# Optimization experiments

Measured on AMD Instinct MI355X. Metric: run time of the kernel, lower is better.

## Reference

```python
import jax, jax.numpy as jnp
import numpy as np

H = 300  # hidden size hardcoded in the module
VX = 32000
VY = 32000
NX, NY, B = 128, 128, 256


def setup_inputs() -> dict:
    key = jax.random.key(0)
    ks = jax.random.split(key, 10)
    s = 1.0 / np.sqrt(H)
    x = jax.random.randint(ks[0], (NX, B), 0, VX)
    y = jax.random.randint(ks[1], (NY, B), 0, VY)
    # padding_idx=0: zero the pad row of each embedding table
    enc_emb = jax.random.normal(ks[2], (VX, H), jnp.float32).at[0].set(0.0)
    encW = jax.random.uniform(ks[3], (H, H), jnp.float32, -s, s)
    encb = jax.random.uniform(ks[4], (H,), jnp.float32, -s, s)
    dec_emb = jax.random.normal(ks[5], (VY, H), jnp.float32).at[0].set(0.0)
    decW = jax.random.uniform(ks[6], (H, H), jnp.float32, -s, s)
    decb = jax.random.uniform(ks[7], (H,), jnp.float32, -s, s)
    outW = jax.random.uniform(ks[8], (VY, H), jnp.float32, -s, s)
    outb = jax.random.uniform(ks[9], (VY,), jnp.float32, -s, s)
    return {"x": x, "y": y, "enc_emb": enc_emb, "encW": encW, "encb": encb,
            "dec_emb": dec_emb, "decW": decW, "decb": decb,
            "outW": outW, "outb": outb}


def reference(x, y, enc_emb, encW, encb, dec_emb, decW, decb, outW, outb):
    # Encoder: Elman recurrence h = relu(e_x[i] + W h + b)
    e_x = enc_emb[x]                                  # [NX, B, H]
    h0 = jnp.zeros((x.shape[1], H), e_x.dtype)        # h=0 broadcast over batch

    def enc_step(h, ex):
        return jax.nn.relu(ex + h @ encW.T + encb), None

    h, _ = jax.lax.scan(enc_step, h0, e_x)

    # Decoder: teacher-forced recurrence with per-step mean cross-entropy
    e_y = dec_emb[y]                                  # [NY, B, H]

    def dec_step(h, inp):
        ey, tgt = inp
        h = jax.nn.relu(ey + h @ decW.T + decb)
        logits = h @ outW.T + outb                    # [B, VY]
        logp = jax.nn.log_softmax(logits, axis=-1)
        ce = -jnp.mean(jnp.take_along_axis(logp, tgt[:, None], axis=-1))
        return h, ce

    _, ces = jax.lax.scan(dec_step, h, (e_y[:-1], y[1:]))
    return jnp.sum(ces)
```

## Files before the change

### kernel.cpp

```cpp
#include <hip/hip_runtime.h>
#include <hip/hip_bf16.h>
#include <stdint.h>

typedef unsigned short u16;
typedef unsigned char u8;
typedef float f32x4 __attribute__((ext_vector_type(4)));
typedef float f32x2 __attribute__((ext_vector_type(2)));
typedef _Float16 f16x2 __attribute__((ext_vector_type(2)));
typedef _Float16 f16x8 __attribute__((ext_vector_type(8)));

#define H      300
#define KP     320
#define BATCH  256
#define NX     128
#define NY     128
#define VY     32000
#define NPAD   32768
#define MROWS  32512


#define OWS_OFF   0UL
#define OWS_BYTES ((unsigned long)NPAD * KP)
#define OWS_PAD   131072UL
#define A8_OFF    (OWS_OFF + OWS_BYTES + OWS_PAD)
#define A8_BYTES  ((unsigned long)MROWS * KP)
#define WTE_OFF   (A8_OFF + A8_BYTES)
#define WT_BYTES  (320UL * KP * 4)
#define WTD_OFF   (WTE_OFF + WT_BYTES)
#define OBP_OFF   (WTD_OFF + WT_BYTES)
#define OBP_BYTES ((unsigned long)NPAD * 4)
#define SE_OFF    (OBP_OFF + OBP_BYTES)
#define SE_BYTES  ((unsigned long)MROWS * 4)

#define ASYNC_COPY16(dst_lds, src_glb)                                          \
    __builtin_amdgcn_global_load_lds(                                           \
        (const __attribute__((address_space(1))) unsigned int*)(src_glb),       \
        (__attribute__((address_space(3))) unsigned int*)(dst_lds), 16, 0, 0)

__global__ __launch_bounds__(256) void k0_prep(const float* __restrict__ outW,
                                               const float* __restrict__ encW,
                                               const float* __restrict__ decW,
                                               const float* __restrict__ outb,
                                               u8* __restrict__ ows,
                                               float* __restrict__ eob,
                                               float* __restrict__ wte,
                                               float* __restrict__ wtd) {
    long id = (long)blockIdx.x * 256 + threadIdx.x;
    const long n1 = (long)NPAD * KP / 4;
    if (id < n1) {
        int v = (int)(id / 80), k4 = (int)(id % 80) * 4;
        float4 f = {0.f, 0.f, 0.f, 0.f};
        if (v < VY && k4 < H) f = *(const float4*)&outW[(long)v * H + k4];
        int w = __builtin_amdgcn_cvt_pk_fp8_f32(f.x, f.y, 0, false);
        w = __builtin_amdgcn_cvt_pk_fp8_f32(f.z, f.w, w, true);
        long dst = (long)(v >> 6) * 20480 + (k4 >> 5) * 2048 + ((v >> 4) & 3) * 512
                 + (v & 15) * 8 + ((k4 >> 3) & 3) * 128 + (k4 & 7);
        *(unsigned int*)(ows + dst) = (unsigned int)w;
        return;
    }
    long id2 = id - n1;
    if (id2 < NPAD) {
        eob[id2] = (id2 < VY) ? __expf(outb[id2]) : 0.f;
        return;
    }
    id2 -= NPAD;
    if (id2 < 320L * KP) {
        int k = (int)(id2 / KP), j = (int)(id2 % KP);
        wte[id2] = (k < H && j < H) ? encW[j * H + k] : 0.f;
        return;
    }
    id2 -= 320L * KP;
    if (id2 < 320L * KP) {
        int k = (int)(id2 / KP), j = (int)(id2 % KP);
        wtd[id2] = (k < H && j < H) ? decW[j * H + k] : 0.f;
    }
}

__global__ __launch_bounds__(640) void k1_rnn(const int* __restrict__ x,
                                              const int* __restrict__ y,
                                              const float* __restrict__ enc_emb,
                                              const float* __restrict__ dec_emb,
                                              const float* __restrict__ encb,
                                              const float* __restrict__ decb,
                                              const float* __restrict__ wte,
                                              const float* __restrict__ wtd,
                                              u8* __restrict__ A8) {
    const int tid = threadIdx.x;
    const int s = tid / 160;
    const int j = tid - s * 160;
    const int b = blockIdx.x;

    __shared__ __align__(16) _Float16 hh[320];
    __shared__ float part[1280];
    __shared__ __align__(4) u8 a8row[320];

    for (int i = tid; i < 320; i += 640) hh[i] = (_Float16)0.f;

    const bool comb = (tid < 320);
    const int jc = tid;
    const float be = (comb && jc < H) ? encb[jc] : 0.f;
    const float bd = (comb && jc < H) ? decb[jc] : 0.f;

    f16x2 wa[40], wc[40];
#pragma unroll
    for (int kk = 0; kk < 40; ++kk) {
        int k0 = s * 80 + 2 * kk;
        wa[kk] = (f16x2){(_Float16)wte[k0 * KP + j],       (_Float16)wte[(k0 + 1) * KP + j]};
        wc[kk] = (f16x2){(_Float16)wte[k0 * KP + j + 160], (_Float16)wte[(k0 + 1) * KP + j + 160]};
    }

    int idx_n = x[BATCH + b];
    float e_cur = 0.f;
    if (comb && jc < H) e_cur = enc_emb[(long)x[b] * H + jc];
    __syncthreads();

    const f16x8* hb8 = (const f16x8*)&hh[s * 80];

    for (int t = 0; t < NX; ++t) {
        int idx_n2 = x[min(t + 2, NX - 1) * BATCH + b];
        float e_nx = 0.f;
        if (comb && jc < H && t + 1 < NX) e_nx = enc_emb[(long)idx_n * H + jc];

        float p0 = 0.f, p1 = 0.f;
#pragma unroll
        for (int i = 0; i < 10; ++i) {
            f16x8 hv = hb8[i];
            f16x2 q0 = {hv[0], hv[1]}, q1 = {hv[2], hv[3]};
            f16x2 q2 = {hv[4], hv[5]}, q3 = {hv[6], hv[7]};
            p0 = __builtin_amdgcn_fdot2(wa[4 * i + 0], q0, p0, false);
            p1 = __builtin_amdgcn_fdot2(wc[4 * i + 0], q0, p1, false);
            p0 = __builtin_amdgcn_fdot2(wa[4 * i + 1], q1, p0, false);
            p1 = __builtin_amdgcn_fdot2(wc[4 * i + 1], q1, p1, false);
            p0 = __builtin_amdgcn_fdot2(wa[4 * i + 2], q2, p0, false);
            p1 = __builtin_amdgcn_fdot2(wc[4 * i + 2], q2, p1, false);
            p0 = __builtin_amdgcn_fdot2(wa[4 * i + 3], q3, p0, false);
            p1 = __builtin_amdgcn_fdot2(wc[4 * i + 3], q3, p1, false);
        }
        part[s * 320 + j] = p0;
        part[s * 320 + 160 + j] = p1;
        __syncthreads();
        if (comb) {
            float v = part[jc] + part[320 + jc] + part[640 + jc] + part[960 + jc] + be + e_cur;
            hh[jc] = (_Float16)fmaxf(v, 0.f);
        }
        __syncthreads();
        e_cur = e_nx; idx_n = idx_n2;
    }

#pragma unroll
    for (int kk = 0; kk < 40; ++kk) {
        int k0 = s * 80 + 2 * kk;
        wa[kk] = (f16x2){(_Float16)wtd[k0 * KP + j],       (_Float16)wtd[(k0 + 1) * KP + j]};
        wc[kk] = (f16x2){(_Float16)wtd[k0 * KP + j + 160], (_Float16)wtd[(k0 + 1) * KP + j + 160]};
    }

    idx_n = y[BATCH + b];
    e_cur = 0.f;
    if (comb && jc < H) e_cur = dec_emb[(long)y[b] * H + jc];

    for (int t = 0; t < NY - 1; ++t) {
        int idx_n2 = y[min(t + 2, NY - 1) * BATCH + b];
        float e_nx = 0.f;
        if (comb && jc < H && t + 1 < NY - 1) e_nx = dec_emb[(long)idx_n * H + jc];

        float p0 = 0.f, p1 = 0.f;
#pragma unroll
        for (int i = 0; i < 10; ++i) {
            f16x8 hv = hb8[i];
            f16x2 q0 = {hv[0], hv[1]}, q1 = {hv[2], hv[3]};
            f16x2 q2 = {hv[4], hv[5]}, q3 = {hv[6], hv[7]};
            p0 = __builtin_amdgcn_fdot2(wa[4 * i + 0], q0, p0, false);
            p1 = __builtin_amdgcn_fdot2(wc[4 * i + 0], q0, p1, false);
            p0 = __builtin_amdgcn_fdot2(wa[4 * i + 1], q1, p0, false);
            p1 = __builtin_amdgcn_fdot2(wc[4 * i + 1], q1, p1, false);
            p0 = __builtin_amdgcn_fdot2(wa[4 * i + 2], q2, p0, false);
            p1 = __builtin_amdgcn_fdot2(wc[4 * i + 2], q2, p1, false);
            p0 = __builtin_amdgcn_fdot2(wa[4 * i + 3], q3, p0, false);
            p1 = __builtin_amdgcn_fdot2(wc[4 * i + 3], q3, p1, false);
        }
        part[s * 320 + j] = p0;
        part[s * 320 + 160 + j] = p1;
        __syncthreads();
        if (comb) {
            float v = part[jc] + part[320 + jc] + part[640 + jc] + part[960 + jc] + bd + e_cur;
            v = fmaxf(v, 0.f);
            hh[jc] = (_Float16)v;
            int pk = __builtin_amdgcn_cvt_pk_fp8_f32(v, v, 0, false);
            a8row[jc] = (u8)(pk & 0xff);
        }
        __syncthreads();
        if (tid < 80)
            ((unsigned int*)(A8 + (long)(t * BATCH + b) * KP))[tid] =
                ((const unsigned int*)a8row)[tid];
        e_cur = e_nx; idx_n = idx_n2;
    }
}

__global__ __launch_bounds__(256, 2) void k2_gemm(const u8* __restrict__ A8,
                                                  const u8* __restrict__ OWS,
                                                  const float* __restrict__ eob,
                                                  float* __restrict__ sumexp) {
    const int tid = threadIdx.x;
    const int lane = tid & 63, wave = tid >> 6;
    const int lane16 = lane & 15, quad = lane >> 4;
    const int bid = blockIdx.x;
    const int cg8 = bid & 7;
    const int cs  = (bid >> 3) & 3;
    const int rb  = bid >> 5;
    const int colbase = cg8 * 4096 + cs * 1024;
    const long tile0 = (long)(colbase >> 6);

    __shared__ __align__(16) u8 bt[2][20480];

    long a[4][10];
    {
        const u8* abase = A8 + ((long)rb * 256 + wave * 64 + lane16) * KP + quad * 8;
#pragma unroll
        for (int rt = 0; rt < 4; ++rt)
#pragma unroll
            for (int ks = 0; ks < 10; ++ks)
                a[rt][ks] = *(const long*)(abase + rt * 16 * KP + ks * 32);
    }

    {
        const u8* src = OWS + tile0 * 20480 + (wave << 10) + (lane << 4);
        u8* dst = &bt[0][wave << 10];
#pragma unroll
        for (int r = 0; r < 5; ++r)
            ASYNC_COPY16(dst + r * 4096, src + r * 4096);
    }
    __syncthreads();

    float rsum[16];
#pragma unroll
    for (int i = 0; i < 16; ++i) rsum[i] = 0.f;

    for (int ct = 0; ct < 16; ++ct) {
        const u8* bb = &bt[ct & 1][0];

        if (ct < 15) {
            const u8* src = OWS + (tile0 + ct + 1) * 20480 + (wave << 10) + (lane << 4);
            u8* dst = &bt[(ct + 1) & 1][wave << 10];
#pragma unroll
            for (int r = 0; r < 5; ++r)
                ASYNC_COPY16(dst + r * 4096, src + r * 4096);
        }

        f32x4 acc[4][4];
#pragma unroll
        for (int p = 0; p < 4; ++p)
#pragma unroll
            for (int q = 0; q < 4; ++q) acc[p][q] = (f32x4){0.f, 0.f, 0.f, 0.f};

#pragma unroll
        for (int ks = 0; ks < 10; ++ks) {
            long bfr[4];
#pragma unroll
            for (int tc = 0; tc < 4; ++tc)
                bfr[tc] = *(const long*)(bb + ks * 2048 + tc * 512 + lane * 8);
#pragma unroll
            for (int rt = 0; rt < 4; ++rt)
#pragma unroll
                for (int tc = 0; tc < 4; ++tc)
                    acc[rt][tc] = __builtin_amdgcn_mfma_f32_16x16x32_fp8_fp8(
                        a[rt][ks], bfr[tc], acc[rt][tc], 0, 0, 0);
        }

        int cb = colbase + ct * 64;
#pragma unroll
        for (int tc = 0; tc < 4; ++tc) {
            float eb = eob[cb + tc * 16 + lane16];
#pragma unroll
            for (int rt = 0; rt < 4; ++rt)
#pragma unroll
                for (int i = 0; i < 4; ++i)
                    rsum[rt * 4 + i] += __expf(acc[rt][tc][i]) * eb;
        }

        __syncthreads();
    }

#pragma unroll
    for (int m = 1; m < 16; m <<= 1)
#pragma unroll
        for (int i = 0; i < 16; ++i) rsum[i] += __shfl_xor(rsum[i], m, 64);
    if (lane16 == 0) {
        float* sp = &sumexp[(long)rb * 256 + wave * 64];
#pragma unroll
        for (int rt = 0; rt < 4; ++rt)
#pragma unroll
            for (int i = 0; i < 4; ++i)
                atomicAdd(&sp[rt * 16 + quad * 4 + i], rsum[rt * 4 + i]);
    }
}

__global__ __launch_bounds__(256) void k3_ce(const u8* __restrict__ A8,
                                             const u8* __restrict__ OWS,
                                             const float* __restrict__ outb,
                                             const float* __restrict__ sumexp,
                                             const int* __restrict__ y,
                                             float* __restrict__ out) {
    const int wave = threadIdx.x >> 6, lane = threadIdx.x & 63;
    const int r = blockIdx.x * 4 + wave;
    const int t = r >> 8, b = r & 255;
    const int tgt = y[(t + 1) * BATCH + b];
    float s = 0.f;
    if (lane < 40) {
        unsigned long long av = *(const unsigned long long*)(A8 + (long)r * KP + lane * 8);
        long wdst = (long)(tgt >> 6) * 20480 + (lane >> 2) * 2048
                  + ((tgt >> 4) & 3) * 512 + (tgt & 15) * 8 + (lane & 3) * 128;
        unsigned long long wv = *(const unsigned long long*)(OWS + wdst);
        unsigned int a4 = (unsigned int)av, a4h = (unsigned int)(av >> 32);
        unsigned int w4 = (unsigned int)wv, w4h = (unsigned int)(wv >> 32);
        f32x2 al = __builtin_amdgcn_cvt_pk_f32_fp8(a4, false);
        f32x2 ah = __builtin_amdgcn_cvt_pk_f32_fp8(a4, true);
        f32x2 wl = __builtin_amdgcn_cvt_pk_f32_fp8(w4, false);
        f32x2 wh = __builtin_amdgcn_cvt_pk_f32_fp8(w4, true);
        s += al[0] * wl[0] + al[1] * wl[1] + ah[0] * wh[0] + ah[1] * wh[1];
        al = __builtin_amdgcn_cvt_pk_f32_fp8(a4h, false);
        ah = __builtin_amdgcn_cvt_pk_f32_fp8(a4h, true);
        wl = __builtin_amdgcn_cvt_pk_f32_fp8(w4h, false);
        wh = __builtin_amdgcn_cvt_pk_f32_fp8(w4h, true);
        s += al[0] * wl[0] + al[1] * wl[1] + ah[0] * wh[0] + ah[1] * wh[1];
    }
#pragma unroll
    for (int m = 1; m < 64; m <<= 1) s += __shfl_xor(s, m, 64);
    __shared__ float part[4];
    if (lane == 0) part[wave] = logf(sumexp[r]) - (s + outb[tgt]);
    __syncthreads();
    if (threadIdx.x == 0) {
        float tot = part[0] + part[1] + part[2] + part[3];
        atomicAdd(out, tot * (1.0f / 256.0f));
    }
}

extern "C" void kernel_launch(void* const* d_in, const int* in_sizes, int n_in,
                              void* d_out, int out_size, void* d_ws, size_t ws_size,
                              hipStream_t stream) {
    (void)in_sizes; (void)n_in; (void)out_size; (void)ws_size;
    const int*   x       = (const int*)d_in[0];
    const int*   y       = (const int*)d_in[1];
    const float* enc_emb = (const float*)d_in[2];
    const float* encW    = (const float*)d_in[3];
    const float* encb    = (const float*)d_in[4];
    const float* dec_emb = (const float*)d_in[5];
    const float* decW    = (const float*)d_in[6];
    const float* decb    = (const float*)d_in[7];
    const float* outW    = (const float*)d_in[8];
    const float* outb    = (const float*)d_in[9];

    char* ws = (char*)d_ws;
    u8* ows  = (u8*)(ws + OWS_OFF);
    u8* A8   = (u8*)(ws + A8_OFF);
    float* wte    = (float*)(ws + WTE_OFF);
    float* wtd    = (float*)(ws + WTD_OFF);
    float* eob    = (float*)(ws + OBP_OFF);
    float* sumexp = (float*)(ws + SE_OFF);

    hipMemsetAsync(sumexp, 0, SE_BYTES, stream);
    hipMemsetAsync(d_out, 0, sizeof(float), stream);

    long n0 = (long)NPAD * KP / 4 + NPAD + 2L * 320 * KP;
    k0_prep<<<(int)((n0 + 255) / 256), 256, 0, stream>>>(outW, encW, decW, outb,
                                                         ows, eob, wte, wtd);
    k1_rnn<<<256, 640, 0, stream>>>(x, y, enc_emb, dec_emb, encb, decb, wte, wtd, A8);
    k2_gemm<<<127 * 32, 256, 0, stream>>>(A8, ows, eob, sumexp);
    k3_ce<<<8128, 256, 0, stream>>>(A8, ows, outb, sumexp, y, (float*)d_out);
}
```

Baseline: 962.7 us.

## Software-pipeline k2_gemm: overlap exp epilogue of previous tile with next MFMA tile

The column-tile loop in k2_gemm now uses two accumulator sets, so the exp-and-sum epilogue for tile ct-1 runs after the MFMA chain of tile ct. The two phases can then interleave and hide transcendental latency behind matrix work, and the barrier moves to the start of each step. In exchange, register pressure rises from a second 64-float accumulator set, which under launch_bounds(256,2) may cause spills or lower occupancy. An unused shared rowsum array is also added.

```diff
diff --git a/kernel.cpp b/kernel.cpp
--- a/kernel.cpp
+++ b/kernel.cpp
@@ -212,6 +212,9 @@
 
     __shared__ __align__(16) u8 bt[2][20480];
 
+    __shared__ float rowsum[64];
+    if (tid < 64) rowsum[tid] = 0.f;
+
     long a[4][10];
     {
         const u8* abase = A8 + ((long)rb * 256 + wave * 64 + lane16) * KP + quad * 8;
@@ -229,44 +232,66 @@
         for (int r = 0; r < 5; ++r)
             ASYNC_COPY16(dst + r * 4096, src + r * 4096);
     }
-    __syncthreads();
 
     float rsum[16];
 #pragma unroll
     for (int i = 0; i < 16; ++i) rsum[i] = 0.f;
 
-    for (int ct = 0; ct < 16; ++ct) {
-        const u8* bb = &bt[ct & 1][0];
-
-        if (ct < 15) {
-            const u8* src = OWS + (tile0 + ct + 1) * 20480 + (wave << 10) + (lane << 4);
-            u8* dst = &bt[(ct + 1) & 1][wave << 10];
-#pragma unroll
-            for (int r = 0; r < 5; ++r)
-                ASYNC_COPY16(dst + r * 4096, src + r * 4096);
-        }
-
-        f32x4 acc[4][4];
-#pragma unroll
-        for (int p = 0; p < 4; ++p)
-#pragma unroll
-            for (int q = 0; q < 4; ++q) acc[p][q] = (f32x4){0.f, 0.f, 0.f, 0.f};
-
-#pragma unroll
-        for (int ks = 0; ks < 10; ++ks) {
-            long bfr[4];
-#pragma unroll
-            for (int tc = 0; tc < 4; ++tc)
-                bfr[tc] = *(const long*)(bb + ks * 2048 + tc * 512 + lane * 8);
-#pragma unroll
-            for (int rt = 0; rt < 4; ++rt)
-#pragma unroll
-                for (int tc = 0; tc < 4; ++tc)
-                    acc[rt][tc] = __builtin_amdgcn_mfma_f32_16x16x32_fp8_fp8(
-                        a[rt][ks], bfr[tc], acc[rt][tc], 0, 0, 0);
-        }
-
-        int cb = colbase + ct * 64;
+    f32x4 accA[4][4], accB[4][4];
+
+#define DO_CT(CUR, PRV, CT, DO_EPI)                                             \
+    {                                                                           \
+        __syncthreads();                                                        \
+        if ((CT) < 15) {                                                        \
+            const u8* src = OWS + (tile0 + (CT) + 1) * 20480                    \
+                          + (wave << 10) + (lane << 4);                         \
+            u8* dst = &bt[((CT) + 1) & 1][wave << 10];                          \
+            _Pragma("unroll")                                                   \
+            for (int r = 0; r < 5; ++r)                                         \
+                ASYNC_COPY16(dst + r * 4096, src + r * 4096);                   \
+        }                                                                       \
+        const u8* bb = &bt[(CT) & 1][0];                                        \
+        _Pragma("unroll")                                                       \
+        for (int p = 0; p < 4; ++p)                                             \
+            _Pragma("unroll")                                                   \
+            for (int q = 0; q < 4; ++q) CUR[p][q] = (f32x4){0.f, 0.f, 0.f, 0.f};\
+        _Pragma("unroll")                                                       \
+        for (int ks = 0; ks < 10; ++ks) {                                       \
+            long bfr[4];                                                        \
+            _Pragma("unroll")                                                   \
+            for (int tc = 0; tc < 4; ++tc)                                      \
+                bfr[tc] = *(const long*)(bb + ks * 2048 + tc * 512 + lane * 8); \
+            _Pragma("unroll")                                                   \
+            for (int rt = 0; rt < 4; ++rt)                                      \
+                _Pragma("unroll")                                               \
+                for (int tc = 0; tc < 4; ++tc)                                  \
+                    CUR[rt][tc] = __builtin_amdgcn_mfma_f32_16x16x32_fp8_fp8(   \
+                        a[rt][ks], bfr[tc], CUR[rt][tc], 0, 0, 0);              \
+        }                                                                       \
+        if (DO_EPI) {                                                           \
+            int cb = colbase + ((CT) - 1) * 64;                                 \
+            _Pragma("unroll")                                                   \
+            for (int tc = 0; tc < 4; ++tc) {                                    \
+                float eb = eob[cb + tc * 16 + lane16];                          \
+                _Pragma("unroll")                                               \
+                for (int rt = 0; rt < 4; ++rt)                                  \
+                    _Pragma("unroll")                                           \
+                    for (int i = 0; i < 4; ++i)                                 \
+                        rsum[rt * 4 + i] += __expf(PRV[rt][tc][i]) * eb;        \
+            }                                                                   \
+        }                                                                       \
+    }
+
+    DO_CT(accA, accB, 0, false);
+#pragma unroll 1
+    for (int cp = 0; cp < 7; ++cp) {
+        DO_CT(accB, accA, 2 * cp + 1, true);
+        DO_CT(accA, accB, 2 * cp + 2, true);
+    }
+    DO_CT(accB, accA, 15, true);
+
+    {
+        int cb = colbase + 15 * 64;
 #pragma unroll
         for (int tc = 0; tc < 4; ++tc) {
             float eb = eob[cb + tc * 16 + lane16];
@@ -274,11 +299,10 @@
             for (int rt = 0; rt < 4; ++rt)
 #pragma unroll
                 for (int i = 0; i < 4; ++i)
-                    rsum[rt * 4 + i] += __expf(acc[rt][tc][i]) * eb;
-        }
-
-        __syncthreads();
-    }
+                    rsum[rt * 4 + i] += __expf(accB[rt][tc][i]) * eb;
+        }
+    }
+#undef DO_CT
 
 #pragma unroll
     for (int m = 1; m < 16; m <<= 1)
```

After: 1.860 ms. 93.2% more time.

## Software-pipeline exp epilogue with MFMA by splitting accumulators into halves

Applied to the files above, without the earlier changes.

Splits the per-tile 4x4 accumulator set into low and high column halves. The exp-and-sum epilogue of each half now runs while the MFMAs of the other half are issued, so the previous tile's high half overlaps the current tile's low-half MFMAs. The goal is to hide VALU exp work behind matrix-core work rather than running them back to back. The barrier moves to the top of the loop, the loop is marked not to unroll, and a final drain handles the last high half. This adds extra live accumulator registers, which could raise register pressure.

```diff
diff --git a/kernel.cpp b/kernel.cpp
--- a/kernel.cpp
+++ b/kernel.cpp
@@ -229,15 +229,16 @@
         for (int r = 0; r < 5; ++r)
             ASYNC_COPY16(dst + r * 4096, src + r * 4096);
     }
-    __syncthreads();
 
     float rsum[16];
 #pragma unroll
     for (int i = 0; i < 16; ++i) rsum[i] = 0.f;
 
+    f32x4 accLo[4][2], accHi[4][2];
+
+#pragma unroll 1
     for (int ct = 0; ct < 16; ++ct) {
-        const u8* bb = &bt[ct & 1][0];
-
+        __syncthreads();
         if (ct < 15) {
             const u8* src = OWS + (tile0 + ct + 1) * 20480 + (wave << 10) + (lane << 4);
             u8* dst = &bt[(ct + 1) & 1][wave << 10];
@@ -245,39 +246,78 @@
             for (int r = 0; r < 5; ++r)
                 ASYNC_COPY16(dst + r * 4096, src + r * 4096);
         }
-
-        f32x4 acc[4][4];
+        const u8* bb = &bt[ct & 1][0];
+
 #pragma unroll
         for (int p = 0; p < 4; ++p)
 #pragma unroll
-            for (int q = 0; q < 4; ++q) acc[p][q] = (f32x4){0.f, 0.f, 0.f, 0.f};
-
+            for (int q = 0; q < 2; ++q) accLo[p][q] = (f32x4){0.f, 0.f, 0.f, 0.f};
 #pragma unroll
         for (int ks = 0; ks < 10; ++ks) {
-            long bfr[4];
-#pragma unroll
-            for (int tc = 0; tc < 4; ++tc)
-                bfr[tc] = *(const long*)(bb + ks * 2048 + tc * 512 + lane * 8);
+            long b0 = *(const long*)(bb + ks * 2048 + 0 * 512 + lane * 8);
+            long b1 = *(const long*)(bb + ks * 2048 + 1 * 512 + lane * 8);
+#pragma unroll
+            for (int rt = 0; rt < 4; ++rt) {
+                accLo[rt][0] = __builtin_amdgcn_mfma_f32_16x16x32_fp8_fp8(
+                    a[rt][ks], b0, accLo[rt][0], 0, 0, 0);
+                accLo[rt][1] = __builtin_amdgcn_mfma_f32_16x16x32_fp8_fp8(
+                    a[rt][ks], b1, accLo[rt][1], 0, 0, 0);
+            }
+        }
+        if (ct > 0) {
+            int cbp = colbase + (ct - 1) * 64;
+#pragma unroll
+            for (int tc = 0; tc < 2; ++tc) {
+                float eb = eob[cbp + (tc + 2) * 16 + lane16];
+#pragma unroll
+                for (int rt = 0; rt < 4; ++rt)
+#pragma unroll
+                    for (int i = 0; i < 4; ++i)
+                        rsum[rt * 4 + i] += __expf(accHi[rt][tc][i]) * eb;
+            }
+        }
+
+#pragma unroll
+        for (int p = 0; p < 4; ++p)
+#pragma unroll
+            for (int q = 0; q < 2; ++q) accHi[p][q] = (f32x4){0.f, 0.f, 0.f, 0.f};
+#pragma unroll
+        for (int ks = 0; ks < 10; ++ks) {
+            long b2 = *(const long*)(bb + ks * 2048 + 2 * 512 + lane * 8);
+            long b3 = *(const long*)(bb + ks * 2048 + 3 * 512 + lane * 8);
+#pragma unroll
+            for (int rt = 0; rt < 4; ++rt) {
+                accHi[rt][0] = __builtin_amdgcn_mfma_f32_16x16x32_fp8_fp8(
+                    a[rt][ks], b2, accHi[rt][0], 0, 0, 0);
+                accHi[rt][1] = __builtin_amdgcn_mfma_f32_16x16x32_fp8_fp8(
+                    a[rt][ks], b3, accHi[rt][1], 0, 0, 0);
+            }
+        }
+        {
+            int cb = colbase + ct * 64;
+#pragma unroll
+            for (int tc = 0; tc < 2; ++tc) {
+                float eb = eob[cb + tc * 16 + lane16];
+#pragma unroll
+                for (int rt = 0; rt < 4; ++rt)
+#pragma unroll
+                    for (int i = 0; i < 4; ++i)
+                        rsum[rt * 4 + i] += __expf(accLo[rt][tc][i]) * eb;
+            }
+        }
+    }
+
+    {
+        int cb = colbase + 15 * 64;
+#pragma unroll
+        for (int tc = 0; tc < 2; ++tc) {
+            float eb = eob[cb + (tc + 2) * 16 + lane16];
 #pragma unroll
             for (int rt = 0; rt < 4; ++rt)
 #pragma unroll
-                for (int tc = 0; tc < 4; ++tc)
-                    acc[rt][tc] = __builtin_amdgcn_mfma_f32_16x16x32_fp8_fp8(
-                        a[rt][ks], bfr[tc], acc[rt][tc], 0, 0, 0);
-        }
-
-        int cb = colbase + ct * 64;
-#pragma unroll
-        for (int tc = 0; tc < 4; ++tc) {
-            float eb = eob[cb + tc * 16 + lane16];
-#pragma unroll
-            for (int rt = 0; rt < 4; ++rt)
-#pragma unroll
                 for (int i = 0; i < 4; ++i)
-                    rsum[rt * 4 + i] += __expf(acc[rt][tc][i]) * eb;
-        }
-
-        __syncthreads();
+                    rsum[rt * 4 + i] += __expf(accHi[rt][tc][i]) * eb;
+        }
     }
 
 #pragma unroll
```

Measured after the change: 960.0 us. About the same (-0.3%).

## Software-pipeline MFMA and exp epilogue in vocab GEMM, raise occupancy to three

Applied to the files above, without the earlier changes.

Splits each 64-column tile of the fp8 logits GEMM into four 16-column phases with two ping-pong accumulators, so the exp/sum epilogue of one phase is interleaved with the MFMAs of the next. This cuts the accumulator count from 16 to 8 f32x4, which frees registers and allows raising launch bounds to three blocks per CU. The intent is to hide transcendental and VALU latency behind matrix work and improve latency hiding. The barrier moves to the top of each iteration. In exchange there are smaller MFMA batches per LDS read and a risk of register spills at the higher occupancy target.

```diff
diff --git a/kernel.cpp b/kernel.cpp
--- a/kernel.cpp
+++ b/kernel.cpp
@@ -196,7 +196,7 @@
     }
 }
 
-__global__ __launch_bounds__(256, 2) void k2_gemm(const u8* __restrict__ A8,
+__global__ __launch_bounds__(256, 3) void k2_gemm(const u8* __restrict__ A8,
                                                   const u8* __restrict__ OWS,
                                                   const float* __restrict__ eob,
                                                   float* __restrict__ sumexp) {
@@ -229,15 +229,40 @@
         for (int r = 0; r < 5; ++r)
             ASYNC_COPY16(dst + r * 4096, src + r * 4096);
     }
-    __syncthreads();
 
     float rsum[16];
 #pragma unroll
     for (int i = 0; i < 16; ++i) rsum[i] = 0.f;
 
+    f32x4 accA[4], accB[4];
+
+#define MFMA_PH(ACC, TC)                                                        \
+    {                                                                           \
+        _Pragma("unroll")                                                       \
+        for (int p = 0; p < 4; ++p) ACC[p] = (f32x4){0.f, 0.f, 0.f, 0.f};       \
+        _Pragma("unroll")                                                       \
+        for (int ks = 0; ks < 10; ++ks) {                                       \
+            long bf = *(const long*)(bb + ks * 2048 + (TC) * 512 + lane * 8);   \
+            _Pragma("unroll")                                                   \
+            for (int rt = 0; rt < 4; ++rt)                                      \
+                ACC[rt] = __builtin_amdgcn_mfma_f32_16x16x32_fp8_fp8(           \
+                    a[rt][ks], bf, ACC[rt], 0, 0, 0);                           \
+        }                                                                       \
+    }
+
+#define EPI_PH(ACC, CTE, TC)                                                    \
+    {                                                                           \
+        float eb = eob[colbase + (CTE) * 64 + (TC) * 16 + lane16];              \
+        _Pragma("unroll")                                                       \
+        for (int rt = 0; rt < 4; ++rt)                                          \
+            _Pragma("unroll")                                                   \
+            for (int i = 0; i < 4; ++i)                                         \
+                rsum[rt * 4 + i] += __expf(ACC[rt][i]) * eb;                    \
+    }
+
+#pragma unroll 1
     for (int ct = 0; ct < 16; ++ct) {
-        const u8* bb = &bt[ct & 1][0];
-
+        __syncthreads();
         if (ct < 15) {
             const u8* src = OWS + (tile0 + ct + 1) * 20480 + (wave << 10) + (lane << 4);
             u8* dst = &bt[(ct + 1) & 1][wave << 10];
@@ -245,40 +270,17 @@
             for (int r = 0; r < 5; ++r)
                 ASYNC_COPY16(dst + r * 4096, src + r * 4096);
         }
-
-        f32x4 acc[4][4];
-#pragma unroll
-        for (int p = 0; p < 4; ++p)
-#pragma unroll
-            for (int q = 0; q < 4; ++q) acc[p][q] = (f32x4){0.f, 0.f, 0.f, 0.f};
-
-#pragma unroll
-        for (int ks = 0; ks < 10; ++ks) {
-            long bfr[4];
-#pragma unroll
-            for (int tc = 0; tc < 4; ++tc)
-                bfr[tc] = *(const long*)(bb + ks * 2048 + tc * 512 + lane * 8);
-#pragma unroll
-            for (int rt = 0; rt < 4; ++rt)
-#pragma unroll
-                for (int tc = 0; tc < 4; ++tc)
-                    acc[rt][tc] = __builtin_amdgcn_mfma_f32_16x16x32_fp8_fp8(
-                        a[rt][ks], bfr[tc], acc[rt][tc], 0, 0, 0);
-        }
-
-        int cb = colbase + ct * 64;
-#pragma unroll
-        for (int tc = 0; tc < 4; ++tc) {
-            float eb = eob[cb + tc * 16 + lane16];
-#pragma unroll
-            for (int rt = 0; rt < 4; ++rt)
-#pragma unroll
-                for (int i = 0; i < 4; ++i)
-                    rsum[rt * 4 + i] += __expf(acc[rt][tc][i]) * eb;
-        }
-
-        __syncthreads();
-    }
+        const u8* bb = &bt[ct & 1][0];
+
+        MFMA_PH(accA, 0); if (ct > 0) EPI_PH(accB, ct - 1, 3);
+        MFMA_PH(accB, 1); EPI_PH(accA, ct, 0);
+        MFMA_PH(accA, 2); EPI_PH(accB, ct, 1);
+        MFMA_PH(accB, 3); EPI_PH(accA, ct, 2);
+    }
+    EPI_PH(accB, 15, 3);
+
+#undef MFMA_PH
+#undef EPI_PH
 
 #pragma unroll
     for (int m = 1; m < 16; m <<= 1)
```

Result: slower. 1.663 ms (+72.8%).
